# Optimization experiments

Measured on AMD Instinct MI355X. Metric: run time of the kernel, lower is better.

The kernel has to match this reference:

```python
import jax, jax.numpy as jnp
import numpy as np

N_NODES = 4096
HID = 64
N_STEP = 10
_OFFSETS = np.array([1, 2, 5, 11, 23, 47, 97, 193])  # circulant graph -> degree 16


def setup_inputs() -> dict:
    rng = np.random.default_rng(0)
    N = N_NODES
    i = np.repeat(np.arange(N), len(_OFFSETS))
    j = (i + np.tile(_OFFSETS, N)) % N
    vals = rng.normal(0.0, 0.5, i.shape).astype(np.float32)
    J = np.zeros((N, N), np.float32)
    J[i, j] = vals
    J[j, i] = vals  # symmetric coupling matrix
    row, col = np.nonzero(J)                      # E directed edges, row-major sorted
    key_fwd = row.astype(np.int64) * N + col
    rev = np.searchsorted(key_fwd, col.astype(np.int64) * N + row)  # reverse-edge index
    ru, cu = np.nonzero(np.triu(J))               # Eu upper-triangular edges
    u2e = np.searchsorted(key_fwd, ru.astype(np.int64) * N + cu)    # upper -> full edge index
    bias = rng.normal(0.0, 0.5, N).astype(np.float32)
    p = lambda *s: jnp.asarray(rng.normal(0.0, 0.1, s).astype(np.float32))
    return {
        'J': jnp.asarray(J), 'bias': jnp.asarray(bias),
        'gat_W': p(4, HID), 'gat_a': p(2 * HID, 1),
        'ci_W1': p(4, HID), 'ci_b1': jnp.zeros((HID,), jnp.float32),
        'ci_W2': p(HID, HID), 'ci_b2': jnp.zeros((HID,), jnp.float32),
        'ci_W3': p(HID, 1), 'ci_b3': jnp.zeros((1,), jnp.float32),
        'row': jnp.asarray(row.astype(np.int32)), 'col': jnp.asarray(col.astype(np.int32)),
        'rev': jnp.asarray(rev.astype(np.int32)),
        'ru': jnp.asarray(ru.astype(np.int32)), 'cu': jnp.asarray(cu.astype(np.int32)),
        'u2e': jnp.asarray(u2e.astype(np.int32)),
        'N_step': N_STEP, 'MPNNtype': 0,
    }


def reference(J, bias, gat_W, gat_a, ci_W1, ci_b1, ci_W2, ci_b2, ci_W3, ci_b3,
              row, col, rev, ru, cu, u2e, N_step, MPNNtype):
    N = J.shape[0]
    adj = (jnp.abs(J) > 0).astype(J.dtype)
    # node features: [-b, b, degree, row-sum of J]
    feat = jnp.stack([-bias, bias, adj.sum(1), J.sum(1)], axis=1)  # [N,4]
    # GAT scores: e[i,j] = leakyrelu([Wh_i || Wh_j] @ a) = leakyrelu(Wh_i@a1 + Wh_j@a2)
    Wh = feat @ gat_W                                  # [N,H]
    f1 = Wh @ gat_a[:HID, 0]
    f2 = Wh @ gat_a[HID:, 0]
    e = jax.nn.leaky_relu(f1[:, None] + f2[None, :], 0.2)
    att = jnp.where(adj > 0, jnp.exp(e), 0.0)
    Cij_matrix = 0.5 * (att + att.T)                   # [N,N]
    Cij_e = Cij_matrix[row, col]                       # [E]
    # Ci readout MLP
    h = jax.nn.relu(feat @ ci_W1 + ci_b1)
    h = jax.nn.relu(h @ ci_W2 + ci_b2)
    Ci = h @ ci_W3 + ci_b3                             # [N,1]
    dom = Ci + Cij_matrix.sum(1, keepdims=True)
    dom = jnp.sign(dom) * jnp.maximum(jnp.abs(dom), 0.1)  # clamp |.| >= 0.1
    bias_scale = bias / dom[:, 0]
    bx_scale = jnp.stack([-bias_scale, bias_scale], axis=1)  # [N,2]
    Jv = J[row, col]
    Jxy_scale = jnp.stack([jnp.stack([Jv, -Jv], -1),
                           jnp.stack([-Jv, Jv], -1)], axis=1) / Cij_e[:, None, None]  # [E,2,2]

    def node_update(em):
        # node_messages[j,:] = sum over edges (i->j) of em[e,:]
        nm = jax.ops.segment_sum(em, col, num_segments=N) / dom   # [N,2]
        lnZ = jnp.log(jnp.sum(jnp.exp(bx_scale + nm), axis=1, keepdims=True))
        return bx_scale + nm - lnZ, lnZ

    em0 = jnp.zeros((row.shape[0], 2), J.dtype)  # log of all-ones messages
    hidden0, lnZ0 = node_update(em0)

    def bp_step(carry, _):
        em, hidden, lnZ = carry
        ln_pj = hidden[row][:, :, None]     # [E,2,1]
        ln_zj = lnZ[row][:, :, None]        # [E,1,1]
        ln_mu_ij = em[rev][:, :, None]      # message on reverse edge, [E,2,1]
        M = jnp.exp(Jxy_scale + ln_pj + ln_zj - ln_mu_ij)          # [E,2,2]
        M = M / jnp.sum(jnp.max(M, axis=1), axis=1)[:, None, None]
        em_new = jnp.log(jnp.max(M ** Cij_e[:, None, None], axis=1))  # [E,2]
        hidden_new, lnZ_new = node_update(em_new)
        return (em_new, hidden_new, lnZ_new), None

    (em, hidden, lnZ), _ = jax.lax.scan(bp_step, (em0, hidden0, lnZ0), None, length=N_step)

    readout = jnp.exp(hidden)                           # [N,2]
    Js = J[ru, cu] / Cij_matrix[ru, cu]                 # [Eu]
    Jxy_u = jnp.exp(jnp.stack([jnp.stack([Js, -Js], -1),
                               jnp.stack([-Js, Js], -1)], axis=1))  # [Eu,2,2]
    temp_i = readout[cu] / jnp.exp(em[u2e])             # [Eu,2]
    temp_j = readout[ru] / jnp.exp(em[rev[u2e]])        # [Eu,2]
    pw = Jxy_u * temp_i[:, None, :] * temp_j[:, :, None]
    pw = pw / jnp.sum(pw, axis=(1, 2), keepdims=True)
    readout_pairwise = pw.reshape(-1, 4)                # [Eu,4]
    Cij_u = Cij_matrix[ru, cu]
    node_H = -jnp.sum(readout * jnp.log(readout + 1e-16), axis=1)
    edge_H = -jnp.sum(readout_pairwise * jnp.log(readout_pairwise + 1e-16), axis=1)
    node_entropy = Ci[:, 0] @ jax.lax.stop_gradient(node_H)
    edge_entropy = Cij_u @ jax.lax.stop_gradient(edge_H)
    return (readout, readout_pairwise, node_entropy + edge_entropy,
            node_entropy, edge_entropy, Ci[:, 0], Cij_u, dom)
```

## Files before the change

kernel.cpp:

```cpp
#include <hip/hip_runtime.h>
#include <cstddef>

#define TB    256
#define DEG   16
#define NSTEP 10

__device__ __forceinline__ float lse2(float a, float b) {
    return fmaxf(a, b) + __logf(1.0f + __expf(-fabsf(a - b)));
}

__global__ __launch_bounds__(TB) void k_setup(
    const float* __restrict__ J, const float* __restrict__ bias,
    const float* __restrict__ gat_W, const float* __restrict__ gat_a,
    const float* __restrict__ W1, const float* __restrict__ b1,
    const float* __restrict__ W2, const float* __restrict__ b2,
    const float* __restrict__ W3, const float* __restrict__ b3,
    const int* __restrict__ col, const int* __restrict__ rev, int N,
    int4* __restrict__ edgeP, float2* __restrict__ dbW, float2* __restrict__ uA,
    float2* __restrict__ emA,
    float* __restrict__ ci_out, float* __restrict__ dom_out, float* __restrict__ ent)
{
    __shared__ float sW2[64 * 64];
    __shared__ float sh1[TB / 16][65];
    const int tidb = threadIdx.x;
    const int g = blockIdx.x * TB + tidb;
    const int i = g >> 4, t = g & 15;
    const int lane = tidb & 63;

    for (int k = tidb; k < 64 * 64; k += TB) sW2[k] = W2[k];
    if (g < 3) ent[g] = 0.0f;
    emA[g] = make_float2(0.0f, 0.0f);

    const int j = col[g];
    const float Jv = J[(size_t)i * (size_t)N + (size_t)j];

    float rs = Jv;
    rs += __shfl_xor(rs, 1); rs += __shfl_xor(rs, 2);
    rs += __shfl_xor(rs, 4); rs += __shfl_xor(rs, 8);

    float rsj = 0.0f;
    {
        const int* colj = col + 16 * j;
        const float* Jrow = J + (size_t)j * (size_t)N;
        #pragma unroll 4
        for (int tt = 0; tt < 16; ++tt) rsj += Jrow[colj[tt]];
    }

    const float bi = bias[i], bj = bias[j];

    float s8 = 0.0f;
    if (lane < 8) {
        int k = lane & 3;
        const float* a = gat_a + ((lane < 4) ? 0 : 64);
        for (int h = 0; h < 64; ++h) s8 += gat_W[k * 64 + h] * a[h];
    }
    const float w10 = __shfl(s8, 0), w11 = __shfl(s8, 1), w12 = __shfl(s8, 2), w13 = __shfl(s8, 3);
    const float w20 = __shfl(s8, 4), w21 = __shfl(s8, 5), w22 = __shfl(s8, 6), w23 = __shfl(s8, 7);
    const float fd = (float)DEG;
    const float f1i = -bi * w10 + bi * w11 + fd * w12 + rs  * w13;
    const float f2i = -bi * w20 + bi * w21 + fd * w22 + rs  * w23;
    const float f1j = -bj * w10 + bj * w11 + fd * w12 + rsj * w13;
    const float f2j = -bj * w20 + bj * w21 + fd * w22 + rsj * w23;

    float x1 = f1i + f2j; x1 = (x1 > 0.0f) ? x1 : 0.2f * x1;
    float x2 = f1j + f2i; x2 = (x2 > 0.0f) ? x2 : 0.2f * x2;
    const float C  = 0.5f * (__expf(x1) + __expf(x2));
    const float js = Jv / C;
    edgeP[g] = make_int4(j, rev[g], __float_as_int(js), __float_as_int(C));

    float sc = C;
    sc += __shfl_xor(sc, 1); sc += __shfl_xor(sc, 2);
    sc += __shfl_xor(sc, 4); sc += __shfl_xor(sc, 8);

    const int nib = tidb >> 4;
    __syncthreads();
    #pragma unroll
    for (int m = 0; m < 4; ++m) {
        int h = t + 16 * m;
        float a = -bi * W1[h] + bi * W1[64 + h] + fd * W1[128 + h]
                + rs * W1[192 + h] + b1[h];
        sh1[nib][h] = fmaxf(a, 0.0f);
    }
    __syncthreads();
    float civ = 0.0f;
    #pragma unroll
    for (int m = 0; m < 4; ++m) {
        int o = t + 16 * m;
        float acc = b2[o];
        for (int h = 0; h < 64; ++h) acc += sh1[nib][h] * sW2[h * 64 + o];
        civ += fmaxf(acc, 0.0f) * W3[o];
    }
    civ += __shfl_xor(civ, 1); civ += __shfl_xor(civ, 2);
    civ += __shfl_xor(civ, 4); civ += __shfl_xor(civ, 8);
    const float ci = civ + b3[0];

    const float s  = ci + sc;
    const float cl = fmaxf(fabsf(s), 0.1f);
    const float d  = (s > 0.0f) ? cl : ((s < 0.0f) ? -cl : 0.0f);
    const float bs = bi / d;
    if (t == 0) {
        ci_out[i] = ci; dom_out[i] = d;
        dbW[i] = make_float2(1.0f / d, bs);
        uA[i]  = make_float2(-bs, bs);
    }
}

__global__ __launch_bounds__(TB) void k_step(
    const int4* __restrict__ edgeP, const float2* __restrict__ dbW,
    const float2* __restrict__ uP, const float2* __restrict__ emP,
    float2* __restrict__ uQ, float2* __restrict__ emQ,
    int last, const float* __restrict__ ci_out,
    float2* __restrict__ ro_out, float* __restrict__ ent)
{
    __shared__ float red[TB / 64];
    const int g = blockIdx.x * TB + threadIdx.x;
    const int i = g >> 4, t = g & 15;
    const int4 ep = edgeP[g];
    const int j = ep.x, rg = ep.y;
    const float js = __int_as_float(ep.z), C = __int_as_float(ep.w);

    const float2 uj = uP[j];
    const float2 mu = emP[rg];
    const float a0 = uj.x - mu.x, a1 = uj.y - mu.y;
    const float t0 = fmaxf( js + a0, -js + a1);
    const float t1 = fmaxf(-js + a0,  js + a1);
    const float ls = lse2(t0, t1);
    const float e0 = C * (t0 - ls), e1 = C * (t1 - ls);
    emQ[g] = make_float2(e0, e1);

    float nm0 = e0, nm1 = e1;
    nm0 += __shfl_xor(nm0, 1); nm1 += __shfl_xor(nm1, 1);
    nm0 += __shfl_xor(nm0, 2); nm1 += __shfl_xor(nm1, 2);
    nm0 += __shfl_xor(nm0, 4); nm1 += __shfl_xor(nm1, 4);
    nm0 += __shfl_xor(nm0, 8); nm1 += __shfl_xor(nm1, 8);
    const float2 db = dbW[i];
    const float v0 = -db.y + nm0 * db.x, v1 = db.y + nm1 * db.x;
    if (t == 0) uQ[i] = make_float2(v0, v1);

    if (last) {
        float nodeC = 0.0f;
        if (t == 0) {
            const float lz = lse2(v0, v1);
            const float r0 = __expf(v0 - lz), r1 = __expf(v1 - lz);
            ro_out[i] = make_float2(r0, r1);
            const float H = -(r0 * __logf(r0 + 1e-16f) + r1 * __logf(r1 + 1e-16f));
            nodeC = ci_out[i] * H;
        }
        for (int off = 32; off > 0; off >>= 1) nodeC += __shfl_down(nodeC, off);
        const int lane = threadIdx.x & 63, wv = threadIdx.x >> 6;
        if (lane == 0) red[wv] = nodeC;
        __syncthreads();
        if (threadIdx.x == 0) {
            const float sn = red[0] + red[1] + red[2] + red[3];
            atomicAdd(&ent[0], sn);
            atomicAdd(&ent[1], sn);
        }
    }
}

__global__ __launch_bounds__(TB) void k_epi(
    const int* __restrict__ ru, const int* __restrict__ cu,
    const int* __restrict__ u2e, const int4* __restrict__ edgeP,
    const float2* __restrict__ uF, const float2* __restrict__ emF,
    float4* __restrict__ rp_out, float* __restrict__ cij_out,
    float* __restrict__ ent)
{
    __shared__ float red[TB / 64];
    const int u = blockIdx.x * TB + threadIdx.x;
    const int e = u2e[u], r = ru[u], c = cu[u];
    const int4 ep = edgeP[e];
    const int er = ep.y;
    const float jse = __int_as_float(ep.z), Ce = __int_as_float(ep.w);

    const float2 uc = uF[c], ur = uF[r];
    const float lc = lse2(uc.x, uc.y);
    const float lr = lse2(ur.x, ur.y);
    const float2 eme = emF[er];
    const float2 emr = emF[e];
    const float ti0 = (uc.x - lc) - eme.x, ti1 = (uc.y - lc) - eme.y;
    const float tj0 = (ur.x - lr) - emr.x, tj1 = (ur.y - lr) - emr.y;
    const float L00 =  jse + ti0 + tj0;
    const float L01 = -jse + ti1 + tj0;
    const float L10 = -jse + ti0 + tj1;
    const float L11 =  jse + ti1 + tj1;
    const float mL = fmaxf(fmaxf(L00, L01), fmaxf(L10, L11));
    float p00 = __expf(L00 - mL), p01 = __expf(L01 - mL);
    float p10 = __expf(L10 - mL), p11 = __expf(L11 - mL);
    const float inv = 1.0f / (p00 + p01 + p10 + p11);
    p00 *= inv; p01 *= inv; p10 *= inv; p11 *= inv;
    rp_out[u] = make_float4(p00, p01, p10, p11);
    cij_out[u] = Ce;
    const float H = -(p00 * __logf(p00 + 1e-16f) + p01 * __logf(p01 + 1e-16f)
                    + p10 * __logf(p10 + 1e-16f) + p11 * __logf(p11 + 1e-16f));
    float edgeC = Ce * H;
    for (int off = 32; off > 0; off >>= 1) edgeC += __shfl_down(edgeC, off);
    const int lane = threadIdx.x & 63, wv = threadIdx.x >> 6;
    if (lane == 0) red[wv] = edgeC;
    __syncthreads();
    if (threadIdx.x == 0) {
        const float se = red[0] + red[1] + red[2] + red[3];
        atomicAdd(&ent[0], se);
        atomicAdd(&ent[2], se);
    }
}

extern "C" void kernel_launch(void* const* d_in, const int* in_sizes, int n_in,
                              void* d_out, int out_size, void* d_ws, size_t ws_size,
                              hipStream_t stream) {
    const float* J     = (const float*)d_in[0];
    const float* bias  = (const float*)d_in[1];
    const float* gat_W = (const float*)d_in[2];
    const float* gat_a = (const float*)d_in[3];
    const float* W1    = (const float*)d_in[4];
    const float* b1    = (const float*)d_in[5];
    const float* W2    = (const float*)d_in[6];
    const float* b2    = (const float*)d_in[7];
    const float* W3    = (const float*)d_in[8];
    const float* b3    = (const float*)d_in[9];
    const int*   col   = (const int*)d_in[11];
    const int*   rev   = (const int*)d_in[12];
    const int*   ru    = (const int*)d_in[13];
    const int*   cu    = (const int*)d_in[14];
    const int*   u2e   = (const int*)d_in[15];

    const int N  = in_sizes[1];
    const int E  = in_sizes[10];
    const int Eu = in_sizes[13];

    float* out = (float*)d_out;
    size_t OFF_RP  = 2 * (size_t)N;
    size_t OFF_ENT = OFF_RP + 4 * (size_t)Eu;
    float2* ro_out  = (float2*)out;
    float4* rp_out  = (float4*)(out + OFF_RP);
    float*  ent     = out + OFF_ENT;
    float*  ci_out  = ent + 3;
    float*  cij_out = ci_out + N;
    float*  dom_out = cij_out + Eu;

    char* w = (char*)d_ws;
    auto carve = [&](size_t bytes) {
        void* q = (void*)w;
        w += (bytes + 255) & ~(size_t)255;
        return q;
    };
    int4*   edgeP = (int4*)carve((size_t)E * 16);
    float2* dbW   = (float2*)carve((size_t)N * 8);
    float2* uA    = (float2*)carve((size_t)N * 8);
    float2* uB    = (float2*)carve((size_t)N * 8);
    float2* emA   = (float2*)carve((size_t)E * 8);
    float2* emB   = (float2*)carve((size_t)E * 8);

    const int gE  = E / TB;
    const int gEu = Eu / TB;

    k_setup<<<gE, TB, 0, stream>>>(J, bias, gat_W, gat_a, W1, b1, W2, b2, W3, b3,
                                   col, rev, N, edgeP, dbW, uA, emA,
                                   ci_out, dom_out, ent);

    float2 *uP = uA, *uQ = uB, *emP = emA, *emQ = emB;
    for (int s = 0; s < NSTEP; ++s) {
        const int last = (s == NSTEP - 1) ? 1 : 0;
        k_step<<<gE, TB, 0, stream>>>(edgeP, dbW, uP, emP, uQ, emQ,
                                      last, ci_out, ro_out, ent);
        float2* tp;
        tp = uP;  uP  = uQ;  uQ  = tp;
        tp = emP; emP = emQ; emQ = tp;
    }
    k_epi<<<gEu, TB, 0, stream>>>(ru, cu, u2e, edgeP, uP, emP,
                                  rp_out, cij_out, ent);
}
```

Before: 175.3 us.

## Fuse setup, BP steps and epilogue into one cooperative kernel with grid syncs

Replaces the twelve kernel launches (setup, ten BP steps, epilogue) with a single cooperative kernel that uses grid-wide syncs between phases. Per-edge constants (j, rev, js, C, 1/d, b/d, ci) now stay in registers across steps instead of being reloaded from memory. The neighbour row-sum recomputation is replaced by a node-level f1/f2 table that is read back after a grid sync. Block size doubles to 512, giving 128 blocks, all of which must be co-resident. Launch overhead is traded for grid barrier cost.

```diff
diff --git a/kernel.cpp b/kernel.cpp
--- a/kernel.cpp
+++ b/kernel.cpp
@@ -1,84 +1,72 @@
 #include <hip/hip_runtime.h>
+#include <hip/hip_cooperative_groups.h>
 #include <cstddef>
 
-#define TB    256
-#define DEG   16
+namespace cg = cooperative_groups;
+
+#define TB    512
 #define NSTEP 10
 
 __device__ __forceinline__ float lse2(float a, float b) {
     return fmaxf(a, b) + __logf(1.0f + __expf(-fabsf(a - b)));
 }
 
-__global__ __launch_bounds__(TB) void k_setup(
-    const float* __restrict__ J, const float* __restrict__ bias,
-    const float* __restrict__ gat_W, const float* __restrict__ gat_a,
-    const float* __restrict__ W1, const float* __restrict__ b1,
-    const float* __restrict__ W2, const float* __restrict__ b2,
-    const float* __restrict__ W3, const float* __restrict__ b3,
-    const int* __restrict__ col, const int* __restrict__ rev, int N,
-    int4* __restrict__ edgeP, float2* __restrict__ dbW, float2* __restrict__ uA,
-    float2* __restrict__ emA,
-    float* __restrict__ ci_out, float* __restrict__ dom_out, float* __restrict__ ent)
-{
+struct KParams {
+    const float *J, *bias, *gat_W, *gat_a, *W1, *b1, *W2, *b2, *W3, *b3;
+    const int *col, *rev, *ru, *cu, *u2e;
+    int N, Eu;
+    int4*   edgeP;
+    float2 *fA, *uA, *uB, *emA, *emB;
+    float  *ci_out, *dom_out, *ent;
+    float2* ro_out;
+    float4* rp_out;
+    float*  cij_out;
+};
+
+__global__ __launch_bounds__(TB) void k_fused(KParams p) {
     __shared__ float sW2[64 * 64];
     __shared__ float sh1[TB / 16][65];
+    __shared__ float red[TB / 64];
+    cg::grid_group grid = cg::this_grid();
+
     const int tidb = threadIdx.x;
     const int g = blockIdx.x * TB + tidb;
     const int i = g >> 4, t = g & 15;
     const int lane = tidb & 63;
 
-    for (int k = tidb; k < 64 * 64; k += TB) sW2[k] = W2[k];
-    if (g < 3) ent[g] = 0.0f;
-    emA[g] = make_float2(0.0f, 0.0f);
-
-    const int j = col[g];
-    const float Jv = J[(size_t)i * (size_t)N + (size_t)j];
+    for (int k = tidb; k < 64 * 64; k += TB) sW2[k] = p.W2[k];
+    if (g < 3) p.ent[g] = 0.0f;
+    p.emA[g] = make_float2(0.0f, 0.0f);
+
+    const int j  = p.col[g];
+    const int rg = p.rev[g];
+    const float Jv = p.J[(size_t)i * (size_t)p.N + (size_t)j];
 
     float rs = Jv;
     rs += __shfl_xor(rs, 1); rs += __shfl_xor(rs, 2);
     rs += __shfl_xor(rs, 4); rs += __shfl_xor(rs, 8);
 
-    float rsj = 0.0f;
-    {
-        const int* colj = col + 16 * j;
-        const float* Jrow = J + (size_t)j * (size_t)N;
-        #pragma unroll 4
-        for (int tt = 0; tt < 16; ++tt) rsj += Jrow[colj[tt]];
-    }
-
-    const float bi = bias[i], bj = bias[j];
+    const float bi = p.bias[i];
 
     float s8 = 0.0f;
     if (lane < 8) {
         int k = lane & 3;
-        const float* a = gat_a + ((lane < 4) ? 0 : 64);
-        for (int h = 0; h < 64; ++h) s8 += gat_W[k * 64 + h] * a[h];
+        const float* a = p.gat_a + ((lane < 4) ? 0 : 64);
+        for (int h = 0; h < 64; ++h) s8 += p.gat_W[k * 64 + h] * a[h];
     }
     const float w10 = __shfl(s8, 0), w11 = __shfl(s8, 1), w12 = __shfl(s8, 2), w13 = __shfl(s8, 3);
     const float w20 = __shfl(s8, 4), w21 = __shfl(s8, 5), w22 = __shfl(s8, 6), w23 = __shfl(s8, 7);
-    const float fd = (float)DEG;
-    const float f1i = -bi * w10 + bi * w11 + fd * w12 + rs  * w13;
-    const float f2i = -bi * w20 + bi * w21 + fd * w22 + rs  * w23;
-    const float f1j = -bj * w10 + bj * w11 + fd * w12 + rsj * w13;
-    const float f2j = -bj * w20 + bj * w21 + fd * w22 + rsj * w23;
-
-    float x1 = f1i + f2j; x1 = (x1 > 0.0f) ? x1 : 0.2f * x1;
-    float x2 = f1j + f2i; x2 = (x2 > 0.0f) ? x2 : 0.2f * x2;
-    const float C  = 0.5f * (__expf(x1) + __expf(x2));
-    const float js = Jv / C;
-    edgeP[g] = make_int4(j, rev[g], __float_as_int(js), __float_as_int(C));
-
-    float sc = C;
-    sc += __shfl_xor(sc, 1); sc += __shfl_xor(sc, 2);
-    sc += __shfl_xor(sc, 4); sc += __shfl_xor(sc, 8);
+    const float fd = 16.0f;
+    const float f1i = -bi * w10 + bi * w11 + fd * w12 + rs * w13;
+    const float f2i = -bi * w20 + bi * w21 + fd * w22 + rs * w23;
 
     const int nib = tidb >> 4;
     __syncthreads();
     #pragma unroll
     for (int m = 0; m < 4; ++m) {
         int h = t + 16 * m;
-        float a = -bi * W1[h] + bi * W1[64 + h] + fd * W1[128 + h]
-                + rs * W1[192 + h] + b1[h];
+        float a = -bi * p.W1[h] + bi * p.W1[64 + h] + fd * p.W1[128 + h]
+                + rs * p.W1[192 + h] + p.b1[h];
         sh1[nib][h] = fmaxf(a, 0.0f);
     }
     __syncthreads();
@@ -86,143 +74,135 @@
     #pragma unroll
     for (int m = 0; m < 4; ++m) {
         int o = t + 16 * m;
-        float acc = b2[o];
+        float acc = p.b2[o];
         for (int h = 0; h < 64; ++h) acc += sh1[nib][h] * sW2[h * 64 + o];
-        civ += fmaxf(acc, 0.0f) * W3[o];
+        civ += fmaxf(acc, 0.0f) * p.W3[o];
     }
     civ += __shfl_xor(civ, 1); civ += __shfl_xor(civ, 2);
     civ += __shfl_xor(civ, 4); civ += __shfl_xor(civ, 8);
-    const float ci = civ + b3[0];
-
+    const float ci = civ + p.b3[0];
+
+    if (t == 0) {
+        p.fA[i] = make_float2(f1i, f2i);
+        p.ci_out[i] = ci;
+    }
+    grid.sync();
+
+    const float2 fj = p.fA[j];
+    float x1 = f1i + fj.y; x1 = (x1 > 0.0f) ? x1 : 0.2f * x1;
+    float x2 = fj.x + f2i; x2 = (x2 > 0.0f) ? x2 : 0.2f * x2;
+    const float C  = 0.5f * (__expf(x1) + __expf(x2));
+    const float js = Jv / C;
+    p.edgeP[g] = make_int4(j, rg, __float_as_int(js), __float_as_int(C));
+
+    float sc = C;
+    sc += __shfl_xor(sc, 1); sc += __shfl_xor(sc, 2);
+    sc += __shfl_xor(sc, 4); sc += __shfl_xor(sc, 8);
     const float s  = ci + sc;
     const float cl = fmaxf(fabsf(s), 0.1f);
     const float d  = (s > 0.0f) ? cl : ((s < 0.0f) ? -cl : 0.0f);
-    const float bs = bi / d;
+    const float rd = 1.0f / d;
+    const float bs = bi * rd;
     if (t == 0) {
-        ci_out[i] = ci; dom_out[i] = d;
-        dbW[i] = make_float2(1.0f / d, bs);
-        uA[i]  = make_float2(-bs, bs);
-    }
-}
-
-__global__ __launch_bounds__(TB) void k_step(
-    const int4* __restrict__ edgeP, const float2* __restrict__ dbW,
-    const float2* __restrict__ uP, const float2* __restrict__ emP,
-    float2* __restrict__ uQ, float2* __restrict__ emQ,
-    int last, const float* __restrict__ ci_out,
-    float2* __restrict__ ro_out, float* __restrict__ ent)
-{
-    __shared__ float red[TB / 64];
-    const int g = blockIdx.x * TB + threadIdx.x;
-    const int i = g >> 4, t = g & 15;
-    const int4 ep = edgeP[g];
-    const int j = ep.x, rg = ep.y;
-    const float js = __int_as_float(ep.z), C = __int_as_float(ep.w);
-
-    const float2 uj = uP[j];
-    const float2 mu = emP[rg];
-    const float a0 = uj.x - mu.x, a1 = uj.y - mu.y;
-    const float t0 = fmaxf( js + a0, -js + a1);
-    const float t1 = fmaxf(-js + a0,  js + a1);
-    const float ls = lse2(t0, t1);
-    const float e0 = C * (t0 - ls), e1 = C * (t1 - ls);
-    emQ[g] = make_float2(e0, e1);
-
-    float nm0 = e0, nm1 = e1;
-    nm0 += __shfl_xor(nm0, 1); nm1 += __shfl_xor(nm1, 1);
-    nm0 += __shfl_xor(nm0, 2); nm1 += __shfl_xor(nm1, 2);
-    nm0 += __shfl_xor(nm0, 4); nm1 += __shfl_xor(nm1, 4);
-    nm0 += __shfl_xor(nm0, 8); nm1 += __shfl_xor(nm1, 8);
-    const float2 db = dbW[i];
-    const float v0 = -db.y + nm0 * db.x, v1 = db.y + nm1 * db.x;
-    if (t == 0) uQ[i] = make_float2(v0, v1);
-
-    if (last) {
-        float nodeC = 0.0f;
-        if (t == 0) {
-            const float lz = lse2(v0, v1);
-            const float r0 = __expf(v0 - lz), r1 = __expf(v1 - lz);
-            ro_out[i] = make_float2(r0, r1);
-            const float H = -(r0 * __logf(r0 + 1e-16f) + r1 * __logf(r1 + 1e-16f));
-            nodeC = ci_out[i] * H;
+        p.dom_out[i] = d;
+        p.uA[i] = make_float2(-bs, bs);
+    }
+    grid.sync();
+
+    int eE = 0, eR = 0, eC = 0, eEr = 0;
+    float jse = 0.0f, Ce = 0.0f;
+    if (g < p.Eu) {
+        eE = p.u2e[g]; eR = p.ru[g]; eC = p.cu[g];
+        const int4 ep = p.edgeP[eE];
+        eEr = ep.y; jse = __int_as_float(ep.z); Ce = __int_as_float(ep.w);
+    }
+
+    float2 *uP = p.uA, *uQ = p.uB, *emP = p.emA, *emQ = p.emB;
+    for (int st = 0; st < NSTEP; ++st) {
+        const float2 uj = uP[j];
+        const float2 mu = emP[rg];
+        const float a0 = uj.x - mu.x, a1 = uj.y - mu.y;
+        const float t0 = fmaxf( js + a0, -js + a1);
+        const float t1 = fmaxf(-js + a0,  js + a1);
+        const float ls = lse2(t0, t1);
+        const float e0 = C * (t0 - ls), e1 = C * (t1 - ls);
+        emQ[g] = make_float2(e0, e1);
+
+        float nm0 = e0, nm1 = e1;
+        nm0 += __shfl_xor(nm0, 1); nm1 += __shfl_xor(nm1, 1);
+        nm0 += __shfl_xor(nm0, 2); nm1 += __shfl_xor(nm1, 2);
+        nm0 += __shfl_xor(nm0, 4); nm1 += __shfl_xor(nm1, 4);
+        nm0 += __shfl_xor(nm0, 8); nm1 += __shfl_xor(nm1, 8);
+        const float v0 = -bs + nm0 * rd, v1 = bs + nm1 * rd;
+        if (t == 0) uQ[i] = make_float2(v0, v1);
+
+        if (st == NSTEP - 1) {
+            float nodeC = 0.0f;
+            if (t == 0) {
+                const float lz = lse2(v0, v1);
+                const float r0 = __expf(v0 - lz), r1 = __expf(v1 - lz);
+                p.ro_out[i] = make_float2(r0, r1);
+                const float H = -(r0 * __logf(r0 + 1e-16f) + r1 * __logf(r1 + 1e-16f));
+                nodeC = ci * H;
+            }
+            for (int off = 32; off > 0; off >>= 1) nodeC += __shfl_down(nodeC, off);
+            const int wv = tidb >> 6;
+            if (lane == 0) red[wv] = nodeC;
+            __syncthreads();
+            if (tidb == 0) {
+                float sn = 0.0f;
+                #pragma unroll
+                for (int w = 0; w < TB / 64; ++w) sn += red[w];
+                atomicAdd(&p.ent[0], sn);
+                atomicAdd(&p.ent[1], sn);
+            }
         }
-        for (int off = 32; off > 0; off >>= 1) nodeC += __shfl_down(nodeC, off);
-        const int lane = threadIdx.x & 63, wv = threadIdx.x >> 6;
-        if (lane == 0) red[wv] = nodeC;
-        __syncthreads();
-        if (threadIdx.x == 0) {
-            const float sn = red[0] + red[1] + red[2] + red[3];
-            atomicAdd(&ent[0], sn);
-            atomicAdd(&ent[1], sn);
-        }
-    }
-}
-
-__global__ __launch_bounds__(TB) void k_epi(
-    const int* __restrict__ ru, const int* __restrict__ cu,
-    const int* __restrict__ u2e, const int4* __restrict__ edgeP,
-    const float2* __restrict__ uF, const float2* __restrict__ emF,
-    float4* __restrict__ rp_out, float* __restrict__ cij_out,
-    float* __restrict__ ent)
-{
-    __shared__ float red[TB / 64];
-    const int u = blockIdx.x * TB + threadIdx.x;
-    const int e = u2e[u], r = ru[u], c = cu[u];
-    const int4 ep = edgeP[e];
-    const int er = ep.y;
-    const float jse = __int_as_float(ep.z), Ce = __int_as_float(ep.w);
-
-    const float2 uc = uF[c], ur = uF[r];
-    const float lc = lse2(uc.x, uc.y);
-    const float lr = lse2(ur.x, ur.y);
-    const float2 eme = emF[er];
-    const float2 emr = emF[e];
-    const float ti0 = (uc.x - lc) - eme.x, ti1 = (uc.y - lc) - eme.y;
-    const float tj0 = (ur.x - lr) - emr.x, tj1 = (ur.y - lr) - emr.y;
-    const float L00 =  jse + ti0 + tj0;
-    const float L01 = -jse + ti1 + tj0;
-    const float L10 = -jse + ti0 + tj1;
-    const float L11 =  jse + ti1 + tj1;
-    const float mL = fmaxf(fmaxf(L00, L01), fmaxf(L10, L11));
-    float p00 = __expf(L00 - mL), p01 = __expf(L01 - mL);
-    float p10 = __expf(L10 - mL), p11 = __expf(L11 - mL);
-    const float inv = 1.0f / (p00 + p01 + p10 + p11);
-    p00 *= inv; p01 *= inv; p10 *= inv; p11 *= inv;
-    rp_out[u] = make_float4(p00, p01, p10, p11);
-    cij_out[u] = Ce;
-    const float H = -(p00 * __logf(p00 + 1e-16f) + p01 * __logf(p01 + 1e-16f)
-                    + p10 * __logf(p10 + 1e-16f) + p11 * __logf(p11 + 1e-16f));
-    float edgeC = Ce * H;
+        grid.sync();
+        float2* tp;
+        tp = uP;  uP  = uQ;  uQ  = tp;
+        tp = emP; emP = emQ; emQ = tp;
+    }
+
+    float edgeC = 0.0f;
+    if (g < p.Eu) {
+        const float2 uc = uP[eC], ur = uP[eR];
+        const float lc = lse2(uc.x, uc.y);
+        const float lr = lse2(ur.x, ur.y);
+        const float2 eme = emP[eEr];
+        const float2 emr = emP[eE];
+        const float ti0 = (uc.x - lc) - eme.x, ti1 = (uc.y - lc) - eme.y;
+        const float tj0 = (ur.x - lr) - emr.x, tj1 = (ur.y - lr) - emr.y;
+        const float L00 =  jse + ti0 + tj0;
+        const float L01 = -jse + ti1 + tj0;
+        const float L10 = -jse + ti0 + tj1;
+        const float L11 =  jse + ti1 + tj1;
+        const float mL = fmaxf(fmaxf(L00, L01), fmaxf(L10, L11));
+        float p00 = __expf(L00 - mL), p01 = __expf(L01 - mL);
+        float p10 = __expf(L10 - mL), p11 = __expf(L11 - mL);
+        const float inv = 1.0f / (p00 + p01 + p10 + p11);
+        p00 *= inv; p01 *= inv; p10 *= inv; p11 *= inv;
+        p.rp_out[g] = make_float4(p00, p01, p10, p11);
+        p.cij_out[g] = Ce;
+        const float H = -(p00 * __logf(p00 + 1e-16f) + p01 * __logf(p01 + 1e-16f)
+                        + p10 * __logf(p10 + 1e-16f) + p11 * __logf(p11 + 1e-16f));
+        edgeC = Ce * H;
+    }
     for (int off = 32; off > 0; off >>= 1) edgeC += __shfl_down(edgeC, off);
-    const int lane = threadIdx.x & 63, wv = threadIdx.x >> 6;
+    const int wv = tidb >> 6;
     if (lane == 0) red[wv] = edgeC;
     __syncthreads();
-    if (threadIdx.x == 0) {
-        const float se = red[0] + red[1] + red[2] + red[3];
-        atomicAdd(&ent[0], se);
-        atomicAdd(&ent[2], se);
+    if (tidb == 0) {
+        float se = 0.0f;
+        #pragma unroll
+        for (int w = 0; w < TB / 64; ++w) se += red[w];
+        atomicAdd(&p.ent[0], se);
+        atomicAdd(&p.ent[2], se);
     }
 }
 
 extern "C" void kernel_launch(void* const* d_in, const int* in_sizes, int n_in,
                               void* d_out, int out_size, void* d_ws, size_t ws_size,
                               hipStream_t stream) {
-    const float* J     = (const float*)d_in[0];
-    const float* bias  = (const float*)d_in[1];
-    const float* gat_W = (const float*)d_in[2];
-    const float* gat_a = (const float*)d_in[3];
-    const float* W1    = (const float*)d_in[4];
-    const float* b1    = (const float*)d_in[5];
-    const float* W2    = (const float*)d_in[6];
-    const float* b2    = (const float*)d_in[7];
-    const float* W3    = (const float*)d_in[8];
-    const float* b3    = (const float*)d_in[9];
-    const int*   col   = (const int*)d_in[11];
-    const int*   rev   = (const int*)d_in[12];
-    const int*   ru    = (const int*)d_in[13];
-    const int*   cu    = (const int*)d_in[14];
-    const int*   u2e   = (const int*)d_in[15];
-
     const int N  = in_sizes[1];
     const int E  = in_sizes[10];
     const int Eu = in_sizes[13];
@@ -230,12 +210,6 @@
     float* out = (float*)d_out;
     size_t OFF_RP  = 2 * (size_t)N;
     size_t OFF_ENT = OFF_RP + 4 * (size_t)Eu;
-    float2* ro_out  = (float2*)out;
-    float4* rp_out  = (float4*)(out + OFF_RP);
-    float*  ent     = out + OFF_ENT;
-    float*  ci_out  = ent + 3;
-    float*  cij_out = ci_out + N;
-    float*  dom_out = cij_out + Eu;
 
     char* w = (char*)d_ws;
     auto carve = [&](size_t bytes) {
@@ -243,29 +217,41 @@
         w += (bytes + 255) & ~(size_t)255;
         return q;
     };
-    int4*   edgeP = (int4*)carve((size_t)E * 16);
-    float2* dbW   = (float2*)carve((size_t)N * 8);
-    float2* uA    = (float2*)carve((size_t)N * 8);
-    float2* uB    = (float2*)carve((size_t)N * 8);
-    float2* emA   = (float2*)carve((size_t)E * 8);
-    float2* emB   = (float2*)carve((size_t)E * 8);
-
-    const int gE  = E / TB;
-    const int gEu = Eu / TB;
-
-    k_setup<<<gE, TB, 0, stream>>>(J, bias, gat_W, gat_a, W1, b1, W2, b2, W3, b3,
-                                   col, rev, N, edgeP, dbW, uA, emA,
-                                   ci_out, dom_out, ent);
-
-    float2 *uP = uA, *uQ = uB, *emP = emA, *emQ = emB;
-    for (int s = 0; s < NSTEP; ++s) {
-        const int last = (s == NSTEP - 1) ? 1 : 0;
-        k_step<<<gE, TB, 0, stream>>>(edgeP, dbW, uP, emP, uQ, emQ,
-                                      last, ci_out, ro_out, ent);
-        float2* tp;
-        tp = uP;  uP  = uQ;  uQ  = tp;
-        tp = emP; emP = emQ; emQ = tp;
-    }
-    k_epi<<<gEu, TB, 0, stream>>>(ru, cu, u2e, edgeP, uP, emP,
-                                  rp_out, cij_out, ent);
+
+    KParams p;
+    p.J     = (const float*)d_in[0];
+    p.bias  = (const float*)d_in[1];
+    p.gat_W = (const float*)d_in[2];
+    p.gat_a = (const float*)d_in[3];
+    p.W1    = (const float*)d_in[4];
+    p.b1    = (const float*)d_in[5];
+    p.W2    = (const float*)d_in[6];
+    p.b2    = (const float*)d_in[7];
+    p.W3    = (const float*)d_in[8];
+    p.b3    = (const float*)d_in[9];
+    p.col   = (const int*)d_in[11];
+    p.rev   = (const int*)d_in[12];
+    p.ru    = (const int*)d_in[13];
+    p.cu    = (const int*)d_in[14];
+    p.u2e   = (const int*)d_in[15];
+    p.N = N; p.Eu = Eu;
+
+    p.edgeP = (int4*)carve((size_t)E * 16);
+    p.fA    = (float2*)carve((size_t)N * 8);
+    p.uA    = (float2*)carve((size_t)N * 8);
+    p.uB    = (float2*)carve((size_t)N * 8);
+    p.emA   = (float2*)carve((size_t)E * 8);
+    p.emB   = (float2*)carve((size_t)E * 8);
+
+    p.ro_out  = (float2*)out;
+    p.rp_out  = (float4*)(out + OFF_RP);
+    p.ent     = out + OFF_ENT;
+    p.ci_out  = p.ent + 3;
+    p.cij_out = p.ci_out + N;
+    p.dom_out = p.cij_out + Eu;
+
+    const int nb = E / TB;
+    void* args[] = { (void*)&p };
+    hipLaunchCooperativeKernel((const void*)k_fused, dim3(nb), dim3(TB),
+                               args, 0, stream);
 }
```

Result: slower. 345.7 us (+97.2%).
